# Performance work log

Measured on AMD Instinct MI355X. Metric: run time of the kernel, lower is better.

## Reference

```python
import jax, jax.numpy as jnp
import numpy as np

H = 2048  # hidden_size
B, S = 4, 4096
LEVELS = 3  # hierarchical_compression_levels


def _linear_params(key, out_dim, in_dim):
    kw, kb = jax.random.split(key)
    bound = 1.0 / np.sqrt(in_dim)
    W = jax.random.uniform(kw, (out_dim, in_dim), minval=-bound, maxval=bound, dtype=jnp.float32)
    b = jax.random.uniform(kb, (out_dim,), minval=-bound, maxval=bound, dtype=jnp.float32)
    return W, b


def setup_inputs() -> dict:
    key = jax.random.key(0)
    ks = jax.random.split(key, 12)
    inp = {}
    inp['hidden_states'] = jax.random.normal(ks[0], (B, S, H), dtype=jnp.float32)
    inp['access_frequency'] = jax.random.uniform(ks[1], (B, S), dtype=jnp.float32)
    inp['importance_score'] = jax.random.uniform(ks[2], (B, S), dtype=jnp.float32)
    # compression level 1: H -> H/2 -> H/2 -> H ; level 2: H -> H/4 -> H/4 -> H
    inp['comp1_W'], inp['comp1_b'] = _linear_params(ks[3], H // 2, H)
    inp['adapt1_W'], inp['adapt1_b'] = _linear_params(ks[4], H // 2, H // 2)
    inp['decomp1_W'], inp['decomp1_b'] = _linear_params(ks[5], H, H // 2)
    inp['comp2_W'], inp['comp2_b'] = _linear_params(ks[6], H // 4, H)
    inp['adapt2_W'], inp['adapt2_b'] = _linear_params(ks[7], H // 4, H // 4)
    inp['decomp2_W'], inp['decomp2_b'] = _linear_params(ks[8], H, H // 4)
    # strategy selector: Linear(H, H/4) -> ReLU -> Linear(H/4, LEVELS) -> Softmax
    inp['sel1_W'], inp['sel1_b'] = _linear_params(ks[9], H // 4, H)
    inp['sel2_W'], inp['sel2_b'] = _linear_params(ks[10], LEVELS, H // 4)
    return inp


def reference(hidden_states, access_frequency, importance_score,
              comp1_W, comp1_b, adapt1_W, adapt1_b, decomp1_W, decomp1_b,
              comp2_W, comp2_b, adapt2_W, adapt2_b, decomp2_W, decomp2_b,
              sel1_W, sel1_b, sel2_W, sel2_b):
    h = hidden_states
    h2 = h.shape[-1] // 2
    # _get_compression_strategy: scale first half by freq, second half by importance
    combined = jnp.concatenate(
        [h[..., :h2] * access_frequency[..., None],
         h[..., h2:] * importance_score[..., None]], axis=-1)  # [B,S,H]
    hid = jax.nn.relu(jnp.einsum('bsh,oh->bso', combined, sel1_W) + sel1_b)
    strategy_weights = jax.nn.softmax(jnp.einsum('bso,lo->bsl', hid, sel2_W) + sel2_b, axis=-1)
    selected = jnp.argmax(strategy_weights, axis=-1)  # [B,S] int

    def branch(Wc, bc, Wa, ba, Wd, bd):
        c = jnp.einsum('bsh,oh->bso', h, Wc) + bc          # compress
        c = jnp.einsum('bso,po->bsp', c, Wa) + ba          # frequency adaptor
        return jnp.einsum('bsp,hp->bsh', c, Wd) + bd       # decompress

    out1 = branch(comp1_W, comp1_b, adapt1_W, adapt1_b, decomp1_W, decomp1_b)
    out2 = branch(comp2_W, comp2_b, adapt2_W, adapt2_b, decomp2_W, decomp2_b)
    stacked = jnp.stack([h, out1, out2], axis=2)  # [B,S,LEVELS,H]
    compressed = jnp.take_along_axis(stacked, selected[:, :, None, None], axis=2)[:, :, 0, :]
    return compressed
```

## Files before the change

### kernel.cpp

```cpp
#include <hip/hip_runtime.h>
#include <hip/hip_bf16.h>

#define TOK 16384
#define TAU2 0.001f

typedef __attribute__((ext_vector_type(8))) short short8;
typedef __attribute__((ext_vector_type(4))) float f32x4;

__device__ __forceinline__ unsigned short f32_bf16(float f) {
  __hip_bfloat16 h = __float2bfloat16(f);
  unsigned short u;
  __builtin_memcpy(&u, &h, sizeof(u));
  return u;
}
__device__ __forceinline__ float bf16_f32(unsigned short u) {
  union { unsigned int i; float f; } c; c.i = ((unsigned int)u) << 16; return c.f;
}

__global__ void zero3(int* a, int* c) {
  if (threadIdx.x == 0) { *a = 0; c[0] = 0; c[1] = 0; }
}

__global__ void cvt_kernel(const float* __restrict__ s, unsigned short* __restrict__ d, int n4) {
  int i = blockIdx.x * 256 + threadIdx.x;
  if (i < n4) {
    float4 v = ((const float4*)s)[i];
    union { unsigned short u[4]; uint2 q; } pk;
    pk.u[0] = f32_bf16(v.x); pk.u[1] = f32_bf16(v.y);
    pk.u[2] = f32_bf16(v.z); pk.u[3] = f32_bf16(v.w);
    ((uint2*)d)[i] = pk.q;
  }
}

__global__ void cvt_split_kernel(const float* __restrict__ s,
                                 unsigned short* __restrict__ dhi,
                                 unsigned short* __restrict__ dlo, int n4) {
  int i = blockIdx.x * 256 + threadIdx.x;
  if (i < n4) {
    float4 v = ((const float4*)s)[i];
    const float* f = (const float*)&v;
    union { unsigned short u[4]; uint2 q; } hi, lo;
    #pragma unroll
    for (int e = 0; e < 4; e++) {
      unsigned short h = f32_bf16(f[e]);
      hi.u[e] = h;
      lo.u[e] = f32_bf16(f[e] - bf16_f32(h));
    }
    ((uint2*)dhi)[i] = hi.q;
    ((uint2*)dlo)[i] = lo.q;
  }
}

__global__ void compact_sel(const int* __restrict__ sel, int* __restrict__ idx1,
                            int* __restrict__ idx2, int* __restrict__ cnt) {
  int t = blockIdx.x * 256 + threadIdx.x;
  int s = sel[t];
  if (s == 1) idx1[atomicAdd(&cnt[0], 1)] = t;
  else if (s == 2) idx2[atomicAdd(&cnt[1], 1)] = t;
}

__global__ void pad_idx(int* __restrict__ idx1, int* __restrict__ idx2,
                        const int* __restrict__ cnt, int* __restrict__ mc) {
  const int tid = threadIdx.x;
  const int n1 = cnt[0], n2 = cnt[1];
  const int p1 = (n1 + 127) & ~(int)127, p2 = (n2 + 127) & ~(int)127;
  if (tid < p1 - n1) idx1[n1 + tid] = -1;
  if (tid < p2 - n2) idx2[n2 + tid] = -1;
  if (tid == 0) { mc[0] = p1; mc[1] = p2; }
}

template<int AMODE, int EPI, int AG>
__global__ __launch_bounds__(256, 2)
void gemm_tile(const void* __restrict__ Av,
               const unsigned short* __restrict__ Bw,
               const unsigned short* __restrict__ Bw2,
               const float* __restrict__ bias,
               void* __restrict__ Outv,
               const float* __restrict__ scA, const float* __restrict__ scB,
               const int* __restrict__ idx, const int* __restrict__ mcp,
               int M, int N, int K) {
  __shared__ __align__(16) unsigned short As[(AMODE == 3 ? 2 : 1) * 128 * 32];
  __shared__ __align__(16) unsigned short Bs[(AMODE == 3 ? 2 : 1) * 128 * 32];
  const int LO = 128 * 32;
  const int tid = threadIdx.x;
  const int m0 = blockIdx.y * 128, n0 = blockIdx.x * 128;
  if (mcp && m0 >= *mcp) return;
  const int lane = tid & 63, wave = tid >> 6;
  const int wm = wave >> 1, wn = wave & 1;
  const int quad = lane >> 4, lr = lane & 15;
  const int srow = tid >> 1, scol = (tid & 1) * 16;

  size_t aRowOff;
  {
    int ar = m0 + srow;
    if (AG) { int t = idx[ar]; ar = (t < 0) ? 0 : t; }
    aRowOff = (size_t)ar * K;
  }
  const unsigned short* Brow = Bw + (size_t)(n0 + srow) * K;
  const unsigned short* Brow2 = (AMODE == 3) ? (Bw2 + (size_t)(n0 + srow) * K) : nullptr;

  f32x4 acc[4][4] = {};

  for (int k0 = 0; k0 < K; k0 += 32) {
    if (AMODE == 2) {
      const unsigned short* A = (const unsigned short*)Av;
      const uint4* src = (const uint4*)(A + aRowOff + k0 + scol);
      uint4* dst = (uint4*)(As + srow * 32 + scol);
      dst[0] = src[0]; dst[1] = src[1];
    } else {
      const float* A = (const float*)Av;
      const float4* src = (const float4*)(A + aRowOff + k0 + scol);
      float4 f[4];
      f[0] = src[0]; f[1] = src[1]; f[2] = src[2]; f[3] = src[3];
      float s = 1.0f;
      if (AMODE == 3) {
        int tk = m0 + srow;
        s = ((k0 + scol) * 2 < K) ? scA[tk] : scB[tk];
      }
      union { unsigned short u[16]; uint4 q[2]; } hi;
      union { unsigned short u[16]; uint4 q[2]; } lo;
      const float* ff = (const float*)f;
      #pragma unroll
      for (int e = 0; e < 16; e++) {
        float fv = ff[e];
        if (AMODE == 3) fv *= s;
        unsigned short hb = f32_bf16(fv);
        hi.u[e] = hb;
        if (AMODE == 3) lo.u[e] = f32_bf16(fv - bf16_f32(hb));
      }
      uint4* dst = (uint4*)(As + srow * 32 + scol);
      dst[0] = hi.q[0]; dst[1] = hi.q[1];
      if (AMODE == 3) {
        uint4* dst2 = (uint4*)(As + LO + srow * 32 + scol);
        dst2[0] = lo.q[0]; dst2[1] = lo.q[1];
      }
    }
    {
      const uint4* src = (const uint4*)(Brow + k0 + scol);
      uint4* dst = (uint4*)(Bs + srow * 32 + scol);
      dst[0] = src[0]; dst[1] = src[1];
      if (AMODE == 3) {
        const uint4* src2 = (const uint4*)(Brow2 + k0 + scol);
        uint4* dst2 = (uint4*)(Bs + LO + srow * 32 + scol);
        dst2[0] = src2[0]; dst2[1] = src2[1];
      }
    }
    __syncthreads();
    short8 af[4], bfr[4];
    #pragma unroll
    for (int i = 0; i < 4; i++)
      af[i] = *(const short8*)(As + (wm * 64 + i * 16 + lr) * 32 + quad * 8);
    #pragma unroll
    for (int j = 0; j < 4; j++)
      bfr[j] = *(const short8*)(Bs + (wn * 64 + j * 16 + lr) * 32 + quad * 8);
    if (AMODE == 3) {
      short8 af2[4], bf2[4];
      #pragma unroll
      for (int i = 0; i < 4; i++)
        af2[i] = *(const short8*)(As + LO + (wm * 64 + i * 16 + lr) * 32 + quad * 8);
      #pragma unroll
      for (int j = 0; j < 4; j++)
        bf2[j] = *(const short8*)(Bs + LO + (wn * 64 + j * 16 + lr) * 32 + quad * 8);
      #pragma unroll
      for (int i = 0; i < 4; i++)
        #pragma unroll
        for (int j = 0; j < 4; j++) {
          acc[i][j] = __builtin_amdgcn_mfma_f32_16x16x32_bf16(af[i], bfr[j], acc[i][j], 0, 0, 0);
          acc[i][j] = __builtin_amdgcn_mfma_f32_16x16x32_bf16(af[i], bf2[j], acc[i][j], 0, 0, 0);
          acc[i][j] = __builtin_amdgcn_mfma_f32_16x16x32_bf16(af2[i], bfr[j], acc[i][j], 0, 0, 0);
        }
    } else {
      #pragma unroll
      for (int i = 0; i < 4; i++)
        #pragma unroll
        for (int j = 0; j < 4; j++)
          acc[i][j] = __builtin_amdgcn_mfma_f32_16x16x32_bf16(af[i], bfr[j], acc[i][j], 0, 0, 0);
    }
    __syncthreads();
  }

  #pragma unroll
  for (int i = 0; i < 4; i++) {
    const int rbase = m0 + wm * 64 + i * 16 + quad * 4;
    #pragma unroll
    for (int j = 0; j < 4; j++) {
      const int col = n0 + wn * 64 + j * 16 + lr;
      const float bv = bias[col];
      #pragma unroll
      for (int r = 0; r < 4; r++) {
        const int row = rbase + r;
        float v = acc[i][j][r] + bv;
        if (EPI == 0) {
          ((unsigned short*)Outv)[(size_t)row * N + col] = f32_bf16(v);
        } else if (EPI == 1) {
          ((unsigned short*)Outv)[(size_t)row * N + col] = f32_bf16(fmaxf(v, 0.0f));
        } else if (EPI == 3) {
          ((float*)Outv)[(size_t)row * N + col] = fmaxf(v, 0.0f);
        } else {
          const int t = idx[row];
          if (t >= 0) ((float*)Outv)[(size_t)t * N + col] = v;
        }
      }
    }
  }
}

__global__ __launch_bounds__(256)
void selector_logits_f32(const float* __restrict__ hidf,
                         const float* __restrict__ W2, const float* __restrict__ b2,
                         int* __restrict__ sel, int* __restrict__ risky,
                         int* __restrict__ riskyCount) {
  const int wave = threadIdx.x >> 6, lane = threadIdx.x & 63;
  const int token = blockIdx.x * 4 + wave;
  const float* hs = hidf + (size_t)token * 512 + lane * 8;
  float4 h0 = *(const float4*)hs, h1 = *(const float4*)(hs + 4);
  float p[3];
  #pragma unroll
  for (int c = 0; c < 3; c++) {
    const float* w = W2 + c * 512 + lane * 8;
    float4 w0 = *(const float4*)w, w1 = *(const float4*)(w + 4);
    p[c] = h0.x*w0.x + h0.y*w0.y + h0.z*w0.z + h0.w*w0.w
         + h1.x*w1.x + h1.y*w1.y + h1.z*w1.z + h1.w*w1.w;
  }
  #pragma unroll
  for (int off = 32; off >= 1; off >>= 1) {
    #pragma unroll
    for (int c = 0; c < 3; c++) p[c] += __shfl_xor(p[c], off, 64);
  }
  if (lane == 0) {
    float l0 = p[0] + b2[0], l1 = p[1] + b2[1], l2 = p[2] + b2[2];
    int arg = 0; float best = l0;
    if (l1 > best) { best = l1; arg = 1; }
    if (l2 > best) { best = l2; arg = 2; }
    float second;
    if (arg == 0) second = fmaxf(l1, l2);
    else if (arg == 1) second = fmaxf(l0, l2);
    else second = fmaxf(l0, l1);
    sel[token] = arg;
    if (best - second < TAU2) {
      int idx = atomicAdd(riskyCount, 1);
      risky[idx] = token;
    }
  }
}

__global__ __launch_bounds__(256)
void recheck_exact(const float* __restrict__ h, const float* __restrict__ freq,
                   const float* __restrict__ imp,
                   const float* __restrict__ W1, const float* __restrict__ b1,
                   const float* __restrict__ W2, const float* __restrict__ b2,
                   const int* __restrict__ risky, const int* __restrict__ riskyCount,
                   int* __restrict__ sel) {
  __shared__ float h_sh[2048];
  __shared__ float hid_sh[512];
  const int n = *riskyCount;
  const int tid = threadIdx.x;
  for (int ri = blockIdx.x; ri < n; ri += gridDim.x) {
    const int token = risky[ri];
    {
      const float s = (tid < 128) ? freq[token] : imp[token];
      const float4* src = (const float4*)(h + (size_t)token * 2048) + tid * 2;
      float4 v0 = src[0], v1 = src[1];
      v0.x *= s; v0.y *= s; v0.z *= s; v0.w *= s;
      v1.x *= s; v1.y *= s; v1.z *= s; v1.w *= s;
      ((float4*)h_sh)[tid * 2] = v0;
      ((float4*)h_sh)[tid * 2 + 1] = v1;
    }
    __syncthreads();
    #pragma unroll
    for (int half = 0; half < 2; half++) {
      const int o = tid + half * 256;
      const float* wrow = W1 + (size_t)o * 2048;
      float a0 = 0.f, a1 = 0.f, a2 = 0.f, a3 = 0.f;
      for (int k = 0; k < 2048; k += 16) {
        float4 w0 = *(const float4*)(wrow + k);
        float4 w1v = *(const float4*)(wrow + k + 4);
        float4 w2v = *(const float4*)(wrow + k + 8);
        float4 w3v = *(const float4*)(wrow + k + 12);
        float4 x0 = *(const float4*)(h_sh + k);
        float4 x1 = *(const float4*)(h_sh + k + 4);
        float4 x2 = *(const float4*)(h_sh + k + 8);
        float4 x3 = *(const float4*)(h_sh + k + 12);
        a0 += w0.x*x0.x + w0.y*x0.y + w0.z*x0.z + w0.w*x0.w;
        a1 += w1v.x*x1.x + w1v.y*x1.y + w1v.z*x1.z + w1v.w*x1.w;
        a2 += w2v.x*x2.x + w2v.y*x2.y + w2v.z*x2.z + w2v.w*x2.w;
        a3 += w3v.x*x3.x + w3v.y*x3.y + w3v.z*x3.z + w3v.w*x3.w;
      }
      hid_sh[o] = fmaxf((a0 + a1) + (a2 + a3) + b1[o], 0.0f);
    }
    __syncthreads();
    if (tid < 64) {
      const int lane = tid;
      const float* hs = &hid_sh[lane * 8];
      float l[3];
      #pragma unroll
      for (int c = 0; c < 3; c++) {
        const float* w = W2 + c * 512 + lane * 8;
        float s = 0.0f;
        #pragma unroll
        for (int e = 0; e < 8; e++) s += hs[e] * w[e];
        l[c] = s;
      }
      #pragma unroll
      for (int off = 32; off >= 1; off >>= 1)
        #pragma unroll
        for (int c = 0; c < 3; c++) l[c] += __shfl_xor(l[c], off, 64);
      if (lane == 0) {
        float l0 = l[0] + b2[0], l1 = l[1] + b2[1], l2 = l[2] + b2[2];
        int arg = 0; float best = l0;
        if (l1 > best) { best = l1; arg = 1; }
        if (l2 > best) { arg = 2; }
        sel[token] = arg;
      }
    }
    __syncthreads();
  }
}

__global__ __launch_bounds__(256)
void copy_sel0(const float* __restrict__ h, const int* __restrict__ sel,
               float* __restrict__ out) {
  const int token = blockIdx.x;
  if (sel[token] != 0) return;
  const float4* src = (const float4*)(h + (size_t)token * 2048);
  float4* dst = (float4*)(out + (size_t)token * 2048);
  dst[threadIdx.x] = src[threadIdx.x];
  dst[threadIdx.x + 256] = src[threadIdx.x + 256];
}

extern "C" void kernel_launch(void* const* d_in, const int* in_sizes, int n_in,
                              void* d_out, int out_size, void* d_ws, size_t ws_size,
                              hipStream_t stream) {
  const float* h        = (const float*)d_in[0];
  const float* freq     = (const float*)d_in[1];
  const float* imp      = (const float*)d_in[2];
  const float* comp1W   = (const float*)d_in[3];
  const float* comp1b   = (const float*)d_in[4];
  const float* adapt1W  = (const float*)d_in[5];
  const float* adapt1b  = (const float*)d_in[6];
  const float* decomp1W = (const float*)d_in[7];
  const float* decomp1b = (const float*)d_in[8];
  const float* comp2W   = (const float*)d_in[9];
  const float* comp2b   = (const float*)d_in[10];
  const float* adapt2W  = (const float*)d_in[11];
  const float* adapt2b  = (const float*)d_in[12];
  const float* decomp2W = (const float*)d_in[13];
  const float* decomp2b = (const float*)d_in[14];
  const float* sel1W    = (const float*)d_in[15];
  const float* sel1b    = (const float*)d_in[16];
  const float* sel2W    = (const float*)d_in[17];
  const float* sel2b    = (const float*)d_in[18];
  float* out = (float*)d_out;

  char* ws = (char*)d_ws;
  size_t off = 0;
  auto alloc = [&](size_t bytes) -> void* {
    void* p = ws + off; off += (bytes + 255) & ~(size_t)255; return p;
  };
  unsigned short* wb_comp1   = (unsigned short*)alloc((size_t)1024 * 2048 * 2);
  unsigned short* wb_adapt1  = (unsigned short*)alloc((size_t)1024 * 1024 * 2);
  unsigned short* wb_decomp1 = (unsigned short*)alloc((size_t)2048 * 1024 * 2);
  unsigned short* wb_comp2   = (unsigned short*)alloc((size_t)512 * 2048 * 2);
  unsigned short* wb_adapt2  = (unsigned short*)alloc((size_t)512 * 512 * 2);
  unsigned short* wb_decomp2 = (unsigned short*)alloc((size_t)2048 * 512 * 2);
  unsigned short* w1hi       = (unsigned short*)alloc((size_t)512 * 2048 * 2);
  unsigned short* w1lo       = (unsigned short*)alloc((size_t)512 * 2048 * 2);
  float*          hidf       = (float*)alloc((size_t)TOK * 512 * 4);
  unsigned short* c1         = (unsigned short*)alloc((size_t)TOK * 1024 * 2);
  unsigned short* a1         = (unsigned short*)alloc((size_t)TOK * 1024 * 2);
  int* sel        = (int*)alloc((size_t)TOK * 4);
  int* risky      = (int*)alloc((size_t)TOK * 4);
  int* riskyCount = (int*)alloc(256);
  int* idx1       = (int*)alloc((size_t)TOK * 4);
  int* idx2       = (int*)alloc((size_t)TOK * 4);
  int* cnt        = (int*)alloc(256);
  int* mc         = (int*)alloc(256);
  unsigned short* c2 = c1;
  unsigned short* a2 = a1;

  zero3<<<1, 64, 0, stream>>>(riskyCount, cnt);

  auto cvt = [&](const float* s, unsigned short* d, int n) {
    cvt_kernel<<<(n / 4 + 255) / 256, 256, 0, stream>>>(s, d, n / 4);
  };
  cvt(comp1W,   wb_comp1,   1024 * 2048);
  cvt(adapt1W,  wb_adapt1,  1024 * 1024);
  cvt(decomp1W, wb_decomp1, 2048 * 1024);
  cvt(comp2W,   wb_comp2,   512 * 2048);
  cvt(adapt2W,  wb_adapt2,  512 * 512);
  cvt(decomp2W, wb_decomp2, 2048 * 512);
  cvt_split_kernel<<<(512 * 2048 / 4 + 255) / 256, 256, 0, stream>>>(
      sel1W, w1hi, w1lo, 512 * 2048 / 4);

  gemm_tile<3, 3, 0><<<dim3(512 / 128, TOK / 128), 256, 0, stream>>>(
      h, w1hi, w1lo, sel1b, hidf, freq, imp, nullptr, nullptr, TOK, 512, 2048);
  selector_logits_f32<<<TOK / 4, 256, 0, stream>>>(hidf, sel2W, sel2b, sel, risky, riskyCount);
  recheck_exact<<<256, 256, 0, stream>>>(h, freq, imp, sel1W, sel1b, sel2W, sel2b,
                                         risky, riskyCount, sel);

  compact_sel<<<TOK / 256, 256, 0, stream>>>(sel, idx1, idx2, cnt);
  pad_idx<<<1, 256, 0, stream>>>(idx1, idx2, cnt, mc);

  gemm_tile<0, 0, 1><<<dim3(1024 / 128, TOK / 128), 256, 0, stream>>>(
      h, wb_comp1, nullptr, comp1b, c1, nullptr, nullptr, idx1, mc + 0, TOK, 1024, 2048);
  gemm_tile<2, 0, 0><<<dim3(1024 / 128, TOK / 128), 256, 0, stream>>>(
      c1, wb_adapt1, nullptr, adapt1b, a1, nullptr, nullptr, nullptr, mc + 0, TOK, 1024, 1024);
  gemm_tile<2, 4, 0><<<dim3(2048 / 128, TOK / 128), 256, 0, stream>>>(
      a1, wb_decomp1, nullptr, decomp1b, out, nullptr, nullptr, idx1, mc + 0, TOK, 2048, 1024);

  gemm_tile<0, 0, 1><<<dim3(512 / 128, TOK / 128), 256, 0, stream>>>(
      h, wb_comp2, nullptr, comp2b, c2, nullptr, nullptr, idx2, mc + 1, TOK, 512, 2048);
  gemm_tile<2, 0, 0><<<dim3(512 / 128, TOK / 128), 256, 0, stream>>>(
      c2, wb_adapt2, nullptr, adapt2b, a2, nullptr, nullptr, nullptr, mc + 1, TOK, 512, 512);
  gemm_tile<2, 4, 0><<<dim3(2048 / 128, TOK / 128), 256, 0, stream>>>(
      a2, wb_decomp2, nullptr, decomp2b, out, nullptr, nullptr, idx2, mc + 1, TOK, 2048, 512);

  copy_sel0<<<TOK, 256, 0, stream>>>(h, sel, out);
}
```

Before: 997.3 us.

## Double-buffer branch GEMMs with direct global-to-LDS loads and swizzled tiles

Replaces the generic branch GEMM with a bf16-only kernel. It streams A and B tiles straight into LDS with global_load_lds, double-buffers 64-wide K steps so the next tile loads while the current one is multiplied, and XOR-swizzles LDS chunks to avoid bank conflicts. The hidden states are converted to bf16 once up front, into the output buffer as scratch, so the compress GEMMs no longer convert fp32 per tile. The level-2 intermediates now get their own buffers in the freed selector scratch, and the launches are reordered by stage. The selector GEMM is split into its own kernel and is otherwise unchanged. The extra full conversion pass over the activations adds memory traffic.

```diff
diff --git a/kernel.cpp b/kernel.cpp
--- a/kernel.cpp
+++ b/kernel.cpp
@@ -15,6 +15,12 @@
 }
 __device__ __forceinline__ float bf16_f32(unsigned short u) {
   union { unsigned int i; float f; } c; c.i = ((unsigned int)u) << 16; return c.f;
+}
+
+__device__ __forceinline__ void gll16(const unsigned short* g, unsigned short* l) {
+  __builtin_amdgcn_global_load_lds(
+      (const __attribute__((address_space(1))) unsigned int*)g,
+      (__attribute__((address_space(3))) unsigned int*)l, 16, 0, 0);
 }
 
 __global__ void zero3(int* a, int* c) {
@@ -69,107 +75,71 @@
   if (tid == 0) { mc[0] = p1; mc[1] = p2; }
 }
 
-template<int AMODE, int EPI, int AG>
+template<int EPI, int AG>
 __global__ __launch_bounds__(256, 2)
-void gemm_tile(const void* __restrict__ Av,
+void gemm_bf16(const unsigned short* __restrict__ A,
                const unsigned short* __restrict__ Bw,
-               const unsigned short* __restrict__ Bw2,
                const float* __restrict__ bias,
                void* __restrict__ Outv,
-               const float* __restrict__ scA, const float* __restrict__ scB,
                const int* __restrict__ idx, const int* __restrict__ mcp,
-               int M, int N, int K) {
-  __shared__ __align__(16) unsigned short As[(AMODE == 3 ? 2 : 1) * 128 * 32];
-  __shared__ __align__(16) unsigned short Bs[(AMODE == 3 ? 2 : 1) * 128 * 32];
-  const int LO = 128 * 32;
+               int N, int K) {
+  __shared__ __align__(16) unsigned short As[2][128 * 64];
+  __shared__ __align__(16) unsigned short Bs[2][128 * 64];
   const int tid = threadIdx.x;
   const int m0 = blockIdx.y * 128, n0 = blockIdx.x * 128;
   if (mcp && m0 >= *mcp) return;
   const int lane = tid & 63, wave = tid >> 6;
   const int wm = wave >> 1, wn = wave & 1;
   const int quad = lane >> 4, lr = lane & 15;
-  const int srow = tid >> 1, scol = (tid & 1) * 16;
-
-  size_t aRowOff;
-  {
-    int ar = m0 + srow;
-    if (AG) { int t = idx[ar]; ar = (t < 0) ? 0 : t; }
-    aRowOff = (size_t)ar * K;
-  }
-  const unsigned short* Brow = Bw + (size_t)(n0 + srow) * K;
-  const unsigned short* Brow2 = (AMODE == 3) ? (Bw2 + (size_t)(n0 + srow) * K) : nullptr;
+
+  const int srow = wave * 8 + (lane >> 3);
+  const int schunk = (lane & 7) ^ (lane >> 3);
+  unsigned int aoff[4], boff[4];
+  #pragma unroll
+  for (int r = 0; r < 4; r++) {
+    int row = r * 32 + srow;
+    int gr = m0 + row;
+    if (AG) { int t = idx[gr]; gr = (t < 0) ? 0 : t; }
+    aoff[r] = (unsigned int)gr * (unsigned int)K + (unsigned int)(schunk * 8);
+    boff[r] = (unsigned int)(n0 + row) * (unsigned int)K + (unsigned int)(schunk * 8);
+  }
+  const int lds_dst = (lane & 7) * 8 + (lane >> 3) * 64 + wave * 512;
 
   f32x4 acc[4][4] = {};
-
-  for (int k0 = 0; k0 < K; k0 += 32) {
-    if (AMODE == 2) {
-      const unsigned short* A = (const unsigned short*)Av;
-      const uint4* src = (const uint4*)(A + aRowOff + k0 + scol);
-      uint4* dst = (uint4*)(As + srow * 32 + scol);
-      dst[0] = src[0]; dst[1] = src[1];
-    } else {
-      const float* A = (const float*)Av;
-      const float4* src = (const float4*)(A + aRowOff + k0 + scol);
-      float4 f[4];
-      f[0] = src[0]; f[1] = src[1]; f[2] = src[2]; f[3] = src[3];
-      float s = 1.0f;
-      if (AMODE == 3) {
-        int tk = m0 + srow;
-        s = ((k0 + scol) * 2 < K) ? scA[tk] : scB[tk];
-      }
-      union { unsigned short u[16]; uint4 q[2]; } hi;
-      union { unsigned short u[16]; uint4 q[2]; } lo;
-      const float* ff = (const float*)f;
-      #pragma unroll
-      for (int e = 0; e < 16; e++) {
-        float fv = ff[e];
-        if (AMODE == 3) fv *= s;
-        unsigned short hb = f32_bf16(fv);
-        hi.u[e] = hb;
-        if (AMODE == 3) lo.u[e] = f32_bf16(fv - bf16_f32(hb));
-      }
-      uint4* dst = (uint4*)(As + srow * 32 + scol);
-      dst[0] = hi.q[0]; dst[1] = hi.q[1];
-      if (AMODE == 3) {
-        uint4* dst2 = (uint4*)(As + LO + srow * 32 + scol);
-        dst2[0] = lo.q[0]; dst2[1] = lo.q[1];
-      }
-    }
-    {
-      const uint4* src = (const uint4*)(Brow + k0 + scol);
-      uint4* dst = (uint4*)(Bs + srow * 32 + scol);
-      dst[0] = src[0]; dst[1] = src[1];
-      if (AMODE == 3) {
-        const uint4* src2 = (const uint4*)(Brow2 + k0 + scol);
-        uint4* dst2 = (uint4*)(Bs + LO + srow * 32 + scol);
-        dst2[0] = src2[0]; dst2[1] = src2[1];
-      }
-    }
-    __syncthreads();
-    short8 af[4], bfr[4];
-    #pragma unroll
-    for (int i = 0; i < 4; i++)
-      af[i] = *(const short8*)(As + (wm * 64 + i * 16 + lr) * 32 + quad * 8);
-    #pragma unroll
-    for (int j = 0; j < 4; j++)
-      bfr[j] = *(const short8*)(Bs + (wn * 64 + j * 16 + lr) * 32 + quad * 8);
-    if (AMODE == 3) {
-      short8 af2[4], bf2[4];
-      #pragma unroll
-      for (int i = 0; i < 4; i++)
-        af2[i] = *(const short8*)(As + LO + (wm * 64 + i * 16 + lr) * 32 + quad * 8);
-      #pragma unroll
-      for (int j = 0; j < 4; j++)
-        bf2[j] = *(const short8*)(Bs + LO + (wn * 64 + j * 16 + lr) * 32 + quad * 8);
-      #pragma unroll
-      for (int i = 0; i < 4; i++)
-        #pragma unroll
-        for (int j = 0; j < 4; j++) {
-          acc[i][j] = __builtin_amdgcn_mfma_f32_16x16x32_bf16(af[i], bfr[j], acc[i][j], 0, 0, 0);
-          acc[i][j] = __builtin_amdgcn_mfma_f32_16x16x32_bf16(af[i], bf2[j], acc[i][j], 0, 0, 0);
-          acc[i][j] = __builtin_amdgcn_mfma_f32_16x16x32_bf16(af2[i], bfr[j], acc[i][j], 0, 0, 0);
-        }
-    } else {
+  const int nk = K >> 6;
+
+  #pragma unroll
+  for (int r = 0; r < 4; r++) {
+    gll16(A + aoff[r], &As[0][r * 2048 + lds_dst]);
+    gll16(Bw + boff[r], &Bs[0][r * 2048 + lds_dst]);
+  }
+  __syncthreads();
+
+  int cur = 0;
+  for (int t = 0; t < nk; t++) {
+    if (t + 1 < nk) {
+      const int k0 = (t + 1) << 6;
+      #pragma unroll
+      for (int r = 0; r < 4; r++) {
+        gll16(A + aoff[r] + k0, &As[cur ^ 1][r * 2048 + lds_dst]);
+        gll16(Bw + boff[r] + k0, &Bs[cur ^ 1][r * 2048 + lds_dst]);
+      }
+    }
+    #pragma unroll
+    for (int kk = 0; kk < 2; kk++) {
+      short8 af[4], bfr[4];
+      #pragma unroll
+      for (int i = 0; i < 4; i++) {
+        const int row = wm * 64 + i * 16 + lr;
+        const int c = kk * 4 + quad;
+        af[i] = *(const short8*)(&As[cur][row * 64 + ((c ^ (row & 7)) << 3)]);
+      }
+      #pragma unroll
+      for (int j = 0; j < 4; j++) {
+        const int row = wn * 64 + j * 16 + lr;
+        const int c = kk * 4 + quad;
+        bfr[j] = *(const short8*)(&Bs[cur][row * 64 + ((c ^ (row & 7)) << 3)]);
+      }
       #pragma unroll
       for (int i = 0; i < 4; i++)
         #pragma unroll
@@ -177,6 +147,7 @@
           acc[i][j] = __builtin_amdgcn_mfma_f32_16x16x32_bf16(af[i], bfr[j], acc[i][j], 0, 0, 0);
     }
     __syncthreads();
+    cur ^= 1;
   }
 
   #pragma unroll
@@ -192,14 +163,104 @@
         float v = acc[i][j][r] + bv;
         if (EPI == 0) {
           ((unsigned short*)Outv)[(size_t)row * N + col] = f32_bf16(v);
-        } else if (EPI == 1) {
-          ((unsigned short*)Outv)[(size_t)row * N + col] = f32_bf16(fmaxf(v, 0.0f));
-        } else if (EPI == 3) {
-          ((float*)Outv)[(size_t)row * N + col] = fmaxf(v, 0.0f);
         } else {
-          const int t = idx[row];
-          if (t >= 0) ((float*)Outv)[(size_t)t * N + col] = v;
+          const int tk = idx[row];
+          if (tk >= 0) ((float*)Outv)[(size_t)tk * N + col] = v;
         }
+      }
+    }
+  }
+}
+
+__global__ __launch_bounds__(256, 2)
+void gemm_sel(const float* __restrict__ Af,
+              const unsigned short* __restrict__ Bw,
+              const unsigned short* __restrict__ Bw2,
+              const float* __restrict__ bias,
+              float* __restrict__ Out,
+              const float* __restrict__ scA, const float* __restrict__ scB,
+              int N, int K) {
+  __shared__ __align__(16) unsigned short As[2 * 128 * 32];
+  __shared__ __align__(16) unsigned short Bs[2 * 128 * 32];
+  const int LO = 128 * 32;
+  const int tid = threadIdx.x;
+  const int m0 = blockIdx.y * 128, n0 = blockIdx.x * 128;
+  const int lane = tid & 63, wave = tid >> 6;
+  const int wm = wave >> 1, wn = wave & 1;
+  const int quad = lane >> 4, lr = lane & 15;
+  const int srow = tid >> 1, scol = (tid & 1) * 16;
+
+  const size_t aRowOff = (size_t)(m0 + srow) * K;
+  const unsigned short* Brow = Bw + (size_t)(n0 + srow) * K;
+  const unsigned short* Brow2 = Bw2 + (size_t)(n0 + srow) * K;
+
+  f32x4 acc[4][4] = {};
+
+  for (int k0 = 0; k0 < K; k0 += 32) {
+    {
+      const float4* src = (const float4*)(Af + aRowOff + k0 + scol);
+      float4 f[4];
+      f[0] = src[0]; f[1] = src[1]; f[2] = src[2]; f[3] = src[3];
+      const int tk = m0 + srow;
+      const float s = ((k0 + scol) * 2 < K) ? scA[tk] : scB[tk];
+      union { unsigned short u[16]; uint4 q[2]; } hi;
+      union { unsigned short u[16]; uint4 q[2]; } lo;
+      const float* ff = (const float*)f;
+      #pragma unroll
+      for (int e = 0; e < 16; e++) {
+        float fv = ff[e] * s;
+        unsigned short hb = f32_bf16(fv);
+        hi.u[e] = hb;
+        lo.u[e] = f32_bf16(fv - bf16_f32(hb));
+      }
+      uint4* dst = (uint4*)(As + srow * 32 + scol);
+      dst[0] = hi.q[0]; dst[1] = hi.q[1];
+      uint4* dst2 = (uint4*)(As + LO + srow * 32 + scol);
+      dst2[0] = lo.q[0]; dst2[1] = lo.q[1];
+    }
+    {
+      const uint4* src = (const uint4*)(Brow + k0 + scol);
+      uint4* dst = (uint4*)(Bs + srow * 32 + scol);
+      dst[0] = src[0]; dst[1] = src[1];
+      const uint4* src2 = (const uint4*)(Brow2 + k0 + scol);
+      uint4* dst2 = (uint4*)(Bs + LO + srow * 32 + scol);
+      dst2[0] = src2[0]; dst2[1] = src2[1];
+    }
+    __syncthreads();
+    short8 af[4], bfr[4], af2[4], bf2[4];
+    #pragma unroll
+    for (int i = 0; i < 4; i++) {
+      af[i]  = *(const short8*)(As + (wm * 64 + i * 16 + lr) * 32 + quad * 8);
+      af2[i] = *(const short8*)(As + LO + (wm * 64 + i * 16 + lr) * 32 + quad * 8);
+    }
+    #pragma unroll
+    for (int j = 0; j < 4; j++) {
+      bfr[j] = *(const short8*)(Bs + (wn * 64 + j * 16 + lr) * 32 + quad * 8);
+      bf2[j] = *(const short8*)(Bs + LO + (wn * 64 + j * 16 + lr) * 32 + quad * 8);
+    }
+    #pragma unroll
+    for (int i = 0; i < 4; i++)
+      #pragma unroll
+      for (int j = 0; j < 4; j++) {
+        acc[i][j] = __builtin_amdgcn_mfma_f32_16x16x32_bf16(af[i], bfr[j], acc[i][j], 0, 0, 0);
+        acc[i][j] = __builtin_amdgcn_mfma_f32_16x16x32_bf16(af[i], bf2[j], acc[i][j], 0, 0, 0);
+        acc[i][j] = __builtin_amdgcn_mfma_f32_16x16x32_bf16(af2[i], bfr[j], acc[i][j], 0, 0, 0);
+      }
+    __syncthreads();
+  }
+
+  #pragma unroll
+  for (int i = 0; i < 4; i++) {
+    const int rbase = m0 + wm * 64 + i * 16 + quad * 4;
+    #pragma unroll
+    for (int j = 0; j < 4; j++) {
+      const int col = n0 + wn * 64 + j * 16 + lr;
+      const float bv = bias[col];
+      #pragma unroll
+      for (int r = 0; r < 4; r++) {
+        const int row = rbase + r;
+        float v = acc[i][j][r] + bv;
+        Out[(size_t)row * N + col] = fmaxf(v, 0.0f);
       }
     }
   }
@@ -375,8 +436,10 @@
   int* idx2       = (int*)alloc((size_t)TOK * 4);
   int* cnt        = (int*)alloc(256);
   int* mc         = (int*)alloc(256);
-  unsigned short* c2 = c1;
-  unsigned short* a2 = a1;
+
+  unsigned short* hb = (unsigned short*)out;
+  unsigned short* c2 = (unsigned short*)hidf;
+  unsigned short* a2 = (unsigned short*)hidf + (size_t)TOK * 512;
 
   zero3<<<1, 64, 0, stream>>>(riskyCount, cnt);
 
@@ -389,11 +452,12 @@
   cvt(comp2W,   wb_comp2,   512 * 2048);
   cvt(adapt2W,  wb_adapt2,  512 * 512);
   cvt(decomp2W, wb_decomp2, 2048 * 512);
+  cvt(h,        hb,         TOK * 2048);
   cvt_split_kernel<<<(512 * 2048 / 4 + 255) / 256, 256, 0, stream>>>(
       sel1W, w1hi, w1lo, 512 * 2048 / 4);
 
-  gemm_tile<3, 3, 0><<<dim3(512 / 128, TOK / 128), 256, 0, stream>>>(
-      h, w1hi, w1lo, sel1b, hidf, freq, imp, nullptr, nullptr, TOK, 512, 2048);
+  gemm_sel<<<dim3(512 / 128, TOK / 128), 256, 0, stream>>>(
+      h, w1hi, w1lo, sel1b, hidf, freq, imp, 512, 2048);
   selector_logits_f32<<<TOK / 4, 256, 0, stream>>>(hidf, sel2W, sel2b, sel, risky, riskyCount);
   recheck_exact<<<256, 256, 0, stream>>>(h, freq, imp, sel1W, sel1b, sel2W, sel2b,
                                          risky, riskyCount, sel);
@@ -401,19 +465,18 @@
   compact_sel<<<TOK / 256, 256, 0, stream>>>(sel, idx1, idx2, cnt);
   pad_idx<<<1, 256, 0, stream>>>(idx1, idx2, cnt, mc);
 
-  gemm_tile<0, 0, 1><<<dim3(1024 / 128, TOK / 128), 256, 0, stream>>>(
-      h, wb_comp1, nullptr, comp1b, c1, nullptr, nullptr, idx1, mc + 0, TOK, 1024, 2048);
-  gemm_tile<2, 0, 0><<<dim3(1024 / 128, TOK / 128), 256, 0, stream>>>(
-      c1, wb_adapt1, nullptr, adapt1b, a1, nullptr, nullptr, nullptr, mc + 0, TOK, 1024, 1024);
-  gemm_tile<2, 4, 0><<<dim3(2048 / 128, TOK / 128), 256, 0, stream>>>(
-      a1, wb_decomp1, nullptr, decomp1b, out, nullptr, nullptr, idx1, mc + 0, TOK, 2048, 1024);
-
-  gemm_tile<0, 0, 1><<<dim3(512 / 128, TOK / 128), 256, 0, stream>>>(
-      h, wb_comp2, nullptr, comp2b, c2, nullptr, nullptr, idx2, mc + 1, TOK, 512, 2048);
-  gemm_tile<2, 0, 0><<<dim3(512 / 128, TOK / 128), 256, 0, stream>>>(
-      c2, wb_adapt2, nullptr, adapt2b, a2, nullptr, nullptr, nullptr, mc + 1, TOK, 512, 512);
-  gemm_tile<2, 4, 0><<<dim3(2048 / 128, TOK / 128), 256, 0, stream>>>(
-      a2, wb_decomp2, nullptr, decomp2b, out, nullptr, nullptr, idx2, mc + 1, TOK, 2048, 512);
+  gemm_bf16<0, 1><<<dim3(1024 / 128, TOK / 128), 256, 0, stream>>>(
+      hb, wb_comp1, comp1b, c1, idx1, mc + 0, 1024, 2048);
+  gemm_bf16<0, 1><<<dim3(512 / 128, TOK / 128), 256, 0, stream>>>(
+      hb, wb_comp2, comp2b, c2, idx2, mc + 1, 512, 2048);
+  gemm_bf16<0, 0><<<dim3(1024 / 128, TOK / 128), 256, 0, stream>>>(
+      c1, wb_adapt1, adapt1b, a1, nullptr, mc + 0, 1024, 1024);
+  gemm_bf16<0, 0><<<dim3(512 / 128, TOK / 128), 256, 0, stream>>>(
+      c2, wb_adapt2, adapt2b, a2, nullptr, mc + 1, 512, 512);
+  gemm_bf16<4, 0><<<dim3(2048 / 128, TOK / 128), 256, 0, stream>>>(
+      a1, wb_decomp1, decomp1b, out, idx1, mc + 0, 2048, 1024);
+  gemm_bf16<4, 0><<<dim3(2048 / 128, TOK / 128), 256, 0, stream>>>(
+      a2, wb_decomp2, decomp2b, out, idx2, mc + 1, 2048, 512);
 
   copy_sel0<<<TOK, 256, 0, stream>>>(h, sel, out);
 }
```

Result: no change. 978.4 us (-1.9%).
